# Optimization experiments

Hardware: AMD Instinct MI355X
Metric: run time of the kernel (lower is better)

## Reference

```python
import jax, jax.numpy as jnp
import numpy as np

FS = 24000.0
C_SOUND = 343.0
MAX_TAU = 6
IGNORE = -100
PAIRS = np.array([(0, 1), (0, 2), (0, 3), (1, 2), (1, 3), (2, 3)])  # m1<m2 loop order
PERMS_NP = np.array([(0, 1, 2), (0, 2, 1), (1, 0, 2), (1, 2, 0), (2, 0, 1), (2, 1, 0)])  # itertools order


def _mic_locs():
    # [rad, azi_deg, ele_deg] per mic, centered at origin (matches center_mic_coords)
    coords = np.array([[0.042, 45, 35], [0.042, -45, -35], [0.042, 135, -35], [0.042, -135, 35]], dtype=np.float64)
    rad = coords[:, 0]
    azi = coords[:, 1] * 2 * np.pi / 360
    ele = coords[:, 2] * 2 * np.pi / 360
    locs = np.stack([rad * np.cos(azi) * np.cos(ele), rad * np.sin(azi) * np.cos(ele), rad * np.sin(ele)], axis=1)
    return jnp.asarray(locs, dtype=jnp.float32)

MIC_LOCS = _mic_locs()  # [4,3]


def _get_tdoa_targets(target):
    """Vectorized get_tdoa_target. target: [B,T,E,5,C].
    Assumes <=1 active class per (b,t,track) so the random class shuffle is a no-op.
    Returns (tdoas, tdoas2) as int32 [B,T,E,6]."""
    B, T, E, F, C = target.shape
    active = target[:, :, :, 0, :]                                  # [B,T,E,C] 0/1 flags
    is_active = jnp.any(active > 0, axis=-1)                        # [B,T,E]
    doa = jnp.einsum('btec,btedc->bted', active, target[:, :, :, 1:4, :])  # [B,T,E,3]
    dist = jnp.einsum('btec,btec->bte', active, target[:, :, :, 4, :])     # [B,T,E]
    src = doa * dist[..., None]                                     # [B,T,E,3]
    d = jnp.linalg.norm(src[..., None, :] - MIC_LOCS, axis=-1)      # [B,T,E,4] dist to each mic
    tdoa = d[..., PAIRS[:, 0]] - d[..., PAIRS[:, 1]]                # [B,T,E,6]
    tdoa = jnp.round(tdoa * FS / C_SOUND) + MAX_TAU                 # [B,T,E,6]
    # compact active tracks to the front (stable keeps track order, matching tr_cnt)
    order = jnp.argsort(jnp.logical_not(is_active), axis=-1)        # [B,T,E]
    gathered = jnp.take_along_axis(tdoa, order[..., None], axis=2)  # [B,T,E,6]
    n = jnp.sum(is_active, axis=-1)                                 # [B,T] number of events
    k = jnp.arange(E)[None, None, :]                                # slot index
    idx1 = jnp.clip(jnp.minimum(k, n[:, :, None] - 1), 0, E - 1)    # pad with LAST event
    idx2 = jnp.where(k < n[:, :, None], k, 0)                       # pad with FIRST event
    tdoas = jnp.take_along_axis(gathered, idx1[..., None], axis=2)
    tdoas2 = jnp.take_along_axis(gathered, idx2[..., None], axis=2)
    empty = (n == 0)[:, :, None, None]
    tdoas = jnp.where(empty, float(IGNORE), tdoas)
    tdoas2 = jnp.where(empty, float(IGNORE), tdoas2)
    return tdoas.astype(jnp.int32), tdoas2.astype(jnp.int32)


def _forward(pred, t_a, t_b):
    B, T, C, Tr, ntd = pred.shape
    N = B * T * ntd
    p = pred.transpose(0, 1, 4, 2, 3).reshape(N, C, Tr)             # [N,C,Tr]
    ta = t_a.transpose(0, 1, 3, 2).reshape(N, Tr)                   # [N,Tr]
    tb = t_b.transpose(0, 1, 3, 2).reshape(N, Tr)
    logp = jax.nn.log_softmax(p, axis=1)                            # [N,C,Tr]
    perms = jnp.asarray(PERMS_NP)                                   # [6,Tr]
    ar = jnp.arange(Tr)

    def pit(t):
        tc = jnp.clip(t, 0, C - 1)
        # L[n,i,j] = CE(pred track j, target track i); ignore_index -> 0
        L = -jnp.take_along_axis(logp, jnp.broadcast_to(tc[:, :, None], (N, Tr, Tr)), axis=1)
        L = jnp.where((t == IGNORE)[:, :, None], 0.0, L)
        pl = L[:, ar[None, :], perms].mean(axis=-1)                 # [N,6] per-perm mean loss
        pidx = jnp.argmin(pl, axis=1)                               # first min (matches torch loop)
        return jnp.take_along_axis(pl, pidx[:, None], axis=1)[:, 0], perms[pidx]

    loss1, perm1 = pit(ta)
    loss2, perm2 = pit(tb)
    use2 = loss2 < loss1                                            # torch.min keeps first on ties
    loss = jnp.where(use2, loss2, loss1)
    t_sel = jnp.where(use2[:, None], tb, ta)
    perm_sel = jnp.where(use2[:, None], perm2, perm1)

    pred_cls = jnp.argmax(p, axis=1)                                # [N,Tr]
    t_perm = jnp.take_along_axis(t_sel, perm_sel, axis=1)           # target reordered by opt perm
    valid = t_perm != IGNORE
    npred = jnp.sum(valid)
    correct = jnp.sum((pred_cls == t_perm) & valid)
    acc = jnp.where(npred > 0, correct.astype(jnp.float32) / jnp.maximum(npred, 1).astype(jnp.float32), 0.0)

    mask = loss > 0.0
    nval = jnp.sum(mask)
    lmean = jnp.where(nval > 0, jnp.sum(jnp.where(mask, loss, 0.0)) / jnp.maximum(nval, 1).astype(loss.dtype), 0.0)
    return lmean, acc


def setup_inputs() -> dict:
    key = jax.random.key(0)
    B, T, E, NCLS, NTD, CPRED = 128, 600, 3, 13, 6, 13
    k1, k2, k3, k4, k5 = jax.random.split(key, 5)
    pred = jax.random.normal(k1, (B, T, CPRED, E, NTD), dtype=jnp.float32)
    act_cls = jax.random.randint(k2, (B, T, E), 0, NCLS)
    act_flag = (jax.random.uniform(k3, (B, T, E)) < 0.5).astype(jnp.float32)
    onehot = jax.nn.one_hot(act_cls, NCLS, dtype=jnp.float32) * act_flag[..., None]  # <=1 active class/track
    doa = jax.random.normal(k4, (B, T, E, 3), dtype=jnp.float32)
    doa = doa / jnp.linalg.norm(doa, axis=-1, keepdims=True)
    dist = jax.random.uniform(k5, (B, T, E), minval=1.0, maxval=3.0, dtype=jnp.float32)
    target = jnp.concatenate([
        onehot[:, :, :, None, :],
        jnp.broadcast_to(doa[..., None], (B, T, E, 3, NCLS)),
        jnp.broadcast_to(dist[..., None, None], (B, T, E, 1, NCLS)),
    ], axis=3).astype(jnp.float32)                                  # [B,T,E,5,NCLS]
    return {"pred": pred, "target": target}


def reference(pred, target):
    t_a, t_b = _get_tdoa_targets(target)
    return _forward(pred, t_a, t_b)
```

## Files before the change

### kernel.cpp

```cpp
#include <hip/hip_runtime.h>
#include <cstdint>
#include <cstddef>

#define BT_TOTAL 76800
#define NCLS 13
#define IGN  (-100)

#define CPB   32
#define NBLK  (BT_TOTAL / CPB)
#define ITEMS (CPB * 6)
#define NF4T  (CPB * 195 / 4)
#define KT    7
#define NF4P  (CPB * 234 / 4)
#define KP    8

struct Partial { float ls; int lc; int cor; int val; };

__device__ __forceinline__ void stage16(const float4* __restrict__ g, float4* l) {
    __builtin_amdgcn_global_load_lds((const __attribute__((address_space(1))) void*)g,
                                     (__attribute__((address_space(3))) void*)l,
                                     16, 0, 0);
}

extern "C" __global__ __launch_bounds__(256)
void tdoa_fused(const float* __restrict__ pred, const float* __restrict__ target,
                Partial* __restrict__ part) {
    const int tid = threadIdx.x;
    const int cb  = blockIdx.x * CPB;

    __shared__ float4 sBuf4[NF4P];
    __shared__ uint32_t sTd[CPB * 12];
    const float* sBuf = (const float*)sBuf4;

    {
        const float4* gt = (const float4*)(target + (size_t)cb * 195);
#pragma unroll
        for (int k = 0; k < KT; k++) {
            const int i = k * 256 + tid;
            if (i < NF4T) stage16(gt + i, &sBuf4[i]);
        }
    }
    __syncthreads();

    if (tid < CPB) {
        const float* tg = sBuf + tid * 195;

        const float MX[4] = { 0.02432757455f,  0.02432757455f, -0.02432757455f, -0.02432757455f };
        const float MY[4] = { 0.02432757455f, -0.02432757455f,  0.02432757455f, -0.02432757455f };
        const float MZ[4] = { 0.02409021033f, -0.02409021033f, -0.02409021033f,  0.02409021033f };
        const int PI_[6] = {0,0,0,1,1,2};
        const int PJ_[6] = {1,2,3,2,3,3};

        int  td[3][6];
        bool ab[3];
        int  nact = 0;
#pragma unroll
        for (int e = 0; e < 3; e++) {
            float a[NCLS];
#pragma unroll
            for (int c = 0; c < NCLS; c++) a[c] = tg[e * 65 + c];
            bool ia = false;
#pragma unroll
            for (int c = 0; c < NCLS; c++) ia = ia || (a[c] > 0.0f);
            float d0 = 0.f, d1 = 0.f, d2 = 0.f, ds = 0.f;
#pragma unroll
            for (int c = 0; c < NCLS; c++) {
                d0 += a[c] * tg[e * 65 + 13 + c];
                d1 += a[c] * tg[e * 65 + 26 + c];
                d2 += a[c] * tg[e * 65 + 39 + c];
                ds += a[c] * tg[e * 65 + 52 + c];
            }
            const float sx = d0 * ds, sy = d1 * ds, sz = d2 * ds;
            float dm[4];
#pragma unroll
            for (int m = 0; m < 4; m++) {
                const float ex = sx - MX[m], ey = sy - MY[m], ez = sz - MZ[m];
                dm[m] = sqrtf(ex * ex + ey * ey + ez * ez);
            }
#pragma unroll
            for (int p = 0; p < 6; p++) {
                const float diff = dm[PI_[p]] - dm[PJ_[p]];
                td[e][p] = (int)rintf((diff * 24000.0f) / 343.0f) + 6;
            }
            ab[e] = ia;
            nact += ia ? 1 : 0;
        }

        const int o0 = ab[0] ? 0 : (ab[1] ? 1 : 2);
        const int o1 = (ab[0] && ab[1]) ? 1 : 2;
        const bool empty = (nact == 0);

#pragma unroll
        for (int p = 0; p < 6; p++) {
            const int g0 = (o0 == 0) ? td[0][p] : ((o0 == 1) ? td[1][p] : td[2][p]);
            const int g1 = (o1 == 1) ? td[1][p] : td[2][p];
            const int g2 = td[2][p];
            int ta0 = g0;
            int ta1 = (nact >= 2) ? g1 : g0;
            int ta2 = (nact == 3) ? g2 : ((nact == 2) ? g1 : g0);
            int tb0 = g0;
            int tb1 = (nact >= 2) ? g1 : g0;
            int tb2 = (nact == 3) ? g2 : g0;
            uint32_t w0 = (uint32_t)(ta0 & 0xff) | ((uint32_t)(ta1 & 0xff) << 8) | ((uint32_t)(ta2 & 0xff) << 16);
            uint32_t w1 = (uint32_t)(tb0 & 0xff) | ((uint32_t)(tb1 & 0xff) << 8) | ((uint32_t)(tb2 & 0xff) << 16);
            if (empty) { w0 = 0x009c9c9cu; w1 = 0x009c9c9cu; }
            sTd[tid * 12 + p * 2 + 0] = w0;
            sTd[tid * 12 + p * 2 + 1] = w1;
        }
    }
    __syncthreads();

    {
        const float4* gp = (const float4*)(pred + (size_t)cb * 234);
#pragma unroll
        for (int k = 0; k < KP; k++) {
            const int i = k * 256 + tid;
            if (i < NF4P) stage16(gp + i, &sBuf4[i]);
        }
    }
    __syncthreads();

    float lsum = 0.f;
    int   lcnt = 0, cor = 0, nval = 0;

    if (tid < ITEMS) {
        const int btl = tid / 6;
        const int p   = tid - btl * 6;
        const float* pp = sBuf + btl * 234 + p;

        float x[NCLS][3];
#pragma unroll
        for (int c = 0; c < NCLS; c++)
#pragma unroll
            for (int j = 0; j < 3; j++)
                x[c][j] = pp[c * 18 + j * 6];

        int   am[3];
        float lse[3];
#pragma unroll
        for (int j = 0; j < 3; j++) {
            float m = x[0][j]; int a = 0;
#pragma unroll
            for (int c = 1; c < NCLS; c++) { if (x[c][j] > m) { m = x[c][j]; a = c; } }
            float s = 0.f;
#pragma unroll
            for (int c = 0; c < NCLS; c++) s += expf(x[c][j] - m);
            am[j] = a; lse[j] = m + logf(s);
        }

        const uint32_t w0 = sTd[btl * 12 + p * 2 + 0];
        const uint32_t w1 = sTd[btl * 12 + p * 2 + 1];
        int ta[3], tb[3];
#pragma unroll
        for (int i = 0; i < 3; i++) {
            ta[i] = (int)(int8_t)(w0 >> (8 * i));
            tb[i] = (int)(int8_t)(w1 >> (8 * i));
        }

        float La[3][3], Lb[3][3];
#pragma unroll
        for (int i = 0; i < 3; i++) {
            const int  ca  = (ta[i] < 0) ? 0 : ta[i];
            const int  cb2 = (tb[i] < 0) ? 0 : tb[i];
            const bool ia  = (ta[i] == IGN);
            const bool ib  = (tb[i] == IGN);
#pragma unroll
            for (int j = 0; j < 3; j++) {
                La[i][j] = ia ? 0.f : (lse[j] - pp[ca  * 18 + j * 6]);
                Lb[i][j] = ib ? 0.f : (lse[j] - pp[cb2 * 18 + j * 6]);
            }
        }

        const int P0[6] = {0,0,1,1,2,2};
        const int P1[6] = {1,2,0,2,0,1};
        const int P2[6] = {2,1,2,0,1,0};
        float l1 = 0.f, l2 = 0.f; int i1 = 0, i2 = 0;
#pragma unroll
        for (int q = 0; q < 6; q++) {
            const float va = (La[0][P0[q]] + La[1][P1[q]] + La[2][P2[q]]) * (1.0f / 3.0f);
            const float vb = (Lb[0][P0[q]] + Lb[1][P1[q]] + Lb[2][P2[q]]) * (1.0f / 3.0f);
            if (q == 0) { l1 = va; l2 = vb; }
            else {
                if (va < l1) { l1 = va; i1 = q; }
                if (vb < l2) { l2 = vb; i2 = q; }
            }
        }

        const bool use2 = (l2 < l1);
        const float loss = use2 ? l2 : l1;
        const int  qsel = use2 ? i2 : i1;
        const int PK[6] = {36, 24, 33, 9, 18, 6};
        int pk = PK[0];
#pragma unroll
        for (int k = 1; k < 6; k++) pk = (qsel == k) ? PK[k] : pk;
        const int s0 = use2 ? tb[0] : ta[0];
        const int s1 = use2 ? tb[1] : ta[1];
        const int s2 = use2 ? tb[2] : ta[2];
#pragma unroll
        for (int i = 0; i < 3; i++) {
            const int pi = (pk >> (2 * i)) & 3;
            const int tp = (pi == 0) ? s0 : ((pi == 1) ? s1 : s2);
            const bool v = (tp != IGN);
            nval += v ? 1 : 0;
            cor  += (v && (am[i] == tp)) ? 1 : 0;
        }
        if (loss > 0.f) { lsum += loss; lcnt++; }
    }

#pragma unroll
    for (int off = 32; off > 0; off >>= 1) {
        lsum += __shfl_down(lsum, off, 64);
        lcnt += __shfl_down(lcnt, off, 64);
        cor  += __shfl_down(cor,  off, 64);
        nval += __shfl_down(nval, off, 64);
    }
    __shared__ float rf[4];
    __shared__ int   r1[4], r2[4], r3[4];
    const int wid = tid >> 6;
    if ((tid & 63) == 0) { rf[wid] = lsum; r1[wid] = lcnt; r2[wid] = cor; r3[wid] = nval; }
    __syncthreads();
    if (tid == 0) {
        Partial pt;
        pt.ls  = rf[0] + rf[1] + rf[2] + rf[3];
        pt.lc  = r1[0] + r1[1] + r1[2] + r1[3];
        pt.cor = r2[0] + r2[1] + r2[2] + r2[3];
        pt.val = r3[0] + r3[1] + r3[2] + r3[3];
        part[blockIdx.x] = pt;
    }
}

extern "C" __global__ __launch_bounds__(256)
void tdoa_final(const Partial* __restrict__ part, float* __restrict__ out) {
    const int tid = threadIdx.x;
    double ls = 0.0; int lc = 0, cor = 0, val = 0;
    for (int i = tid; i < NBLK; i += 256) {
        const Partial p = part[i];
        ls += (double)p.ls; lc += p.lc; cor += p.cor; val += p.val;
    }
#pragma unroll
    for (int off = 32; off > 0; off >>= 1) {
        ls  += __shfl_down(ls,  off, 64);
        lc  += __shfl_down(lc,  off, 64);
        cor += __shfl_down(cor, off, 64);
        val += __shfl_down(val, off, 64);
    }
    __shared__ double sd[4];
    __shared__ int    s1[4], s2[4], s3[4];
    const int wid = tid >> 6;
    if ((tid & 63) == 0) { sd[wid] = ls; s1[wid] = lc; s2[wid] = cor; s3[wid] = val; }
    __syncthreads();
    if (tid == 0) {
        const double L = sd[0] + sd[1] + sd[2] + sd[3];
        const int c1 = s1[0] + s1[1] + s1[2] + s1[3];
        const int c2 = s2[0] + s2[1] + s2[2] + s2[3];
        const int c3 = s3[0] + s3[1] + s3[2] + s3[3];
        out[0] = (c1 > 0) ? (float)(L / (double)c1) : 0.0f;
        out[1] = (c3 > 0) ? ((float)c2 / (float)c3) : 0.0f;
    }
}

extern "C" void kernel_launch(void* const* d_in, const int* in_sizes, int n_in,
                              void* d_out, int out_size, void* d_ws, size_t ws_size,
                              hipStream_t stream) {
    const float* pred   = (const float*)d_in[0];
    const float* target = (const float*)d_in[1];
    Partial* part = (Partial*)d_ws;
    float* out = (float*)d_out;
    hipLaunchKernelGGL(tdoa_fused, dim3(NBLK), dim3(256), 0, stream, pred, target, part);
    hipLaunchKernelGGL(tdoa_final, dim3(1),    dim3(256), 0, stream, part, out);
}
```

Before: 152.1 us.

## Issue target and pred loads together and halve block size

Stages both the target and prediction tiles into separate shared buffers up front, so the prediction load no longer waits for the target processing and an extra barrier. Halves the rows per block and the threads per block, which increases the number of blocks and improves latency hiding. This uses more shared memory per row and doubles the partials the final reduction must sum.

```diff
diff --git a/kernel.cpp b/kernel.cpp
--- a/kernel.cpp
+++ b/kernel.cpp
@@ -6,8 +6,9 @@
 #define NCLS 13
 #define IGN  (-100)
 
-#define CPB   32
+#define CPB   16
 #define NBLK  (BT_TOTAL / CPB)
+#define NTHR  128
 #define ITEMS (CPB * 6)
 #define NF4T  (CPB * 195 / 4)
 #define KT    7
@@ -22,28 +23,36 @@
                                      16, 0, 0);
 }
 
-extern "C" __global__ __launch_bounds__(256)
+extern "C" __global__ __launch_bounds__(NTHR)
 void tdoa_fused(const float* __restrict__ pred, const float* __restrict__ target,
                 Partial* __restrict__ part) {
     const int tid = threadIdx.x;
     const int cb  = blockIdx.x * CPB;
 
-    __shared__ float4 sBuf4[NF4P];
+    __shared__ float4 sT4[NF4T];
+    __shared__ float4 sP4[NF4P];
     __shared__ uint32_t sTd[CPB * 12];
-    const float* sBuf = (const float*)sBuf4;
+    const float* sT = (const float*)sT4;
+    const float* sP = (const float*)sP4;
 
     {
         const float4* gt = (const float4*)(target + (size_t)cb * 195);
 #pragma unroll
         for (int k = 0; k < KT; k++) {
-            const int i = k * 256 + tid;
-            if (i < NF4T) stage16(gt + i, &sBuf4[i]);
+            const int i = k * NTHR + tid;
+            if (i < NF4T) stage16(gt + i, &sT4[i]);
+        }
+        const float4* gp = (const float4*)(pred + (size_t)cb * 234);
+#pragma unroll
+        for (int k = 0; k < KP; k++) {
+            const int i = k * NTHR + tid;
+            if (i < NF4P) stage16(gp + i, &sP4[i]);
         }
     }
     __syncthreads();
 
     if (tid < CPB) {
-        const float* tg = sBuf + tid * 195;
+        const float* tg = sT + tid * 195;
 
         const float MX[4] = { 0.02432757455f,  0.02432757455f, -0.02432757455f, -0.02432757455f };
         const float MY[4] = { 0.02432757455f, -0.02432757455f,  0.02432757455f, -0.02432757455f };
@@ -110,23 +119,13 @@
     }
     __syncthreads();
 
-    {
-        const float4* gp = (const float4*)(pred + (size_t)cb * 234);
-#pragma unroll
-        for (int k = 0; k < KP; k++) {
-            const int i = k * 256 + tid;
-            if (i < NF4P) stage16(gp + i, &sBuf4[i]);
-        }
-    }
-    __syncthreads();
-
     float lsum = 0.f;
     int   lcnt = 0, cor = 0, nval = 0;
 
     if (tid < ITEMS) {
         const int btl = tid / 6;
         const int p   = tid - btl * 6;
-        const float* pp = sBuf + btl * 234 + p;
+        const float* pp = sP + btl * 234 + p;
 
         float x[NCLS][3];
 #pragma unroll
@@ -214,17 +213,17 @@
         cor  += __shfl_down(cor,  off, 64);
         nval += __shfl_down(nval, off, 64);
     }
-    __shared__ float rf[4];
-    __shared__ int   r1[4], r2[4], r3[4];
+    __shared__ float rf[2];
+    __shared__ int   r1[2], r2[2], r3[2];
     const int wid = tid >> 6;
     if ((tid & 63) == 0) { rf[wid] = lsum; r1[wid] = lcnt; r2[wid] = cor; r3[wid] = nval; }
     __syncthreads();
     if (tid == 0) {
         Partial pt;
-        pt.ls  = rf[0] + rf[1] + rf[2] + rf[3];
-        pt.lc  = r1[0] + r1[1] + r1[2] + r1[3];
-        pt.cor = r2[0] + r2[1] + r2[2] + r2[3];
-        pt.val = r3[0] + r3[1] + r3[2] + r3[3];
+        pt.ls  = rf[0] + rf[1];
+        pt.lc  = r1[0] + r1[1];
+        pt.cor = r2[0] + r2[1];
+        pt.val = r3[0] + r3[1];
         part[blockIdx.x] = pt;
     }
 }
@@ -266,6 +265,6 @@
     const float* target = (const float*)d_in[1];
     Partial* part = (Partial*)d_ws;
     float* out = (float*)d_out;
-    hipLaunchKernelGGL(tdoa_fused, dim3(NBLK), dim3(256), 0, stream, pred, target, part);
+    hipLaunchKernelGGL(tdoa_fused, dim3(NBLK), dim3(NTHR), 0, stream, pred, target, part);
     hipLaunchKernelGGL(tdoa_final, dim3(1),    dim3(256), 0, stream, part, out);
 }
```

Measured after the change: 164.1 us. +7.9%, slower.

## Flatten kernel to one thread per (cell,pair) reading global memory directly

Applied to the files above, without the earlier changes.

Replaces the block-staged design (async global-to-LDS copies, a 32-thread TDOA phase, and barriers) with a flat grid where every thread handles one (cell, pair) item and reads target and pred straight from global memory. Each thread recomputes only its own pair's TDOA. It also swaps the 13-class dot products for a select of the single active class, which relies on the one-hot assumption. The aim is to drop the barriers and idle lanes. The cost is redundant, uncoalesced strided global reads of target across the 6 threads of a cell, relying on cache for reuse.

```diff
diff --git a/kernel.cpp b/kernel.cpp
--- a/kernel.cpp
+++ b/kernel.cpp
@@ -3,209 +3,145 @@
 #include <cstddef>
 
 #define BT_TOTAL 76800
-#define NCLS 13
-#define IGN  (-100)
-
-#define CPB   32
-#define NBLK  (BT_TOTAL / CPB)
-#define ITEMS (CPB * 6)
-#define NF4T  (CPB * 195 / 4)
-#define KT    7
-#define NF4P  (CPB * 234 / 4)
-#define KP    8
+#define NITEMS   (BT_TOTAL * 6)
+#define NTHR     256
+#define NBLK     (NITEMS / NTHR)
+#define NCLS     13
+#define IGN      (-100)
 
 struct Partial { float ls; int lc; int cor; int val; };
 
-__device__ __forceinline__ void stage16(const float4* __restrict__ g, float4* l) {
-    __builtin_amdgcn_global_load_lds((const __attribute__((address_space(1))) void*)g,
-                                     (__attribute__((address_space(3))) void*)l,
-                                     16, 0, 0);
-}
-
-extern "C" __global__ __launch_bounds__(256)
-void tdoa_fused(const float* __restrict__ pred, const float* __restrict__ target,
-                Partial* __restrict__ part) {
-    const int tid = threadIdx.x;
-    const int cb  = blockIdx.x * CPB;
-
-    __shared__ float4 sBuf4[NF4P];
-    __shared__ uint32_t sTd[CPB * 12];
-    const float* sBuf = (const float*)sBuf4;
-
-    {
-        const float4* gt = (const float4*)(target + (size_t)cb * 195);
-#pragma unroll
-        for (int k = 0; k < KT; k++) {
-            const int i = k * 256 + tid;
-            if (i < NF4T) stage16(gt + i, &sBuf4[i]);
+extern "C" __global__ __launch_bounds__(NTHR, 5)
+void tdoa_flat(const float* __restrict__ pred, const float* __restrict__ target,
+               Partial* __restrict__ part) {
+    const int tid  = threadIdx.x;
+    const int gid  = blockIdx.x * NTHR + tid;
+    const int cell = gid / 6;
+    const int p    = gid - cell * 6;
+
+    const float* tg = target + (size_t)cell * 195;
+    const float* pp = pred   + (size_t)cell * 234 + p;
+
+    const float MX[4] = { 0.02432757455f,  0.02432757455f, -0.02432757455f, -0.02432757455f };
+    const float MY[4] = { 0.02432757455f, -0.02432757455f,  0.02432757455f, -0.02432757455f };
+    const float MZ[4] = { 0.02409021033f, -0.02409021033f, -0.02409021033f,  0.02409021033f };
+    const int PI_[6] = {0,0,0,1,1,2};
+    const int PJ_[6] = {1,2,3,2,3,3};
+    const int mi = PI_[p], mj = PJ_[p];
+    const float mxi = MX[mi], myi = MY[mi], mzi = MZ[mi];
+    const float mxj = MX[mj], myj = MY[mj], mzj = MZ[mj];
+
+    int  td[3];
+    bool ab[3];
+    int  nact = 0;
+#pragma unroll
+    for (int e = 0; e < 3; e++) {
+        float av = 0.f; int ci = 0; bool ia = false;
+#pragma unroll
+        for (int c = 0; c < NCLS; c++) {
+            const float a = tg[e * 65 + c];
+            const bool  g = (a > 0.0f);
+            av = g ? a : av;
+            ci = g ? c : ci;
+            ia = ia || g;
         }
-    }
-    __syncthreads();
-
-    if (tid < CPB) {
-        const float* tg = sBuf + tid * 195;
-
-        const float MX[4] = { 0.02432757455f,  0.02432757455f, -0.02432757455f, -0.02432757455f };
-        const float MY[4] = { 0.02432757455f, -0.02432757455f,  0.02432757455f, -0.02432757455f };
-        const float MZ[4] = { 0.02409021033f, -0.02409021033f, -0.02409021033f,  0.02409021033f };
-        const int PI_[6] = {0,0,0,1,1,2};
-        const int PJ_[6] = {1,2,3,2,3,3};
-
-        int  td[3][6];
-        bool ab[3];
-        int  nact = 0;
-#pragma unroll
-        for (int e = 0; e < 3; e++) {
-            float a[NCLS];
-#pragma unroll
-            for (int c = 0; c < NCLS; c++) a[c] = tg[e * 65 + c];
-            bool ia = false;
-#pragma unroll
-            for (int c = 0; c < NCLS; c++) ia = ia || (a[c] > 0.0f);
-            float d0 = 0.f, d1 = 0.f, d2 = 0.f, ds = 0.f;
-#pragma unroll
-            for (int c = 0; c < NCLS; c++) {
-                d0 += a[c] * tg[e * 65 + 13 + c];
-                d1 += a[c] * tg[e * 65 + 26 + c];
-                d2 += a[c] * tg[e * 65 + 39 + c];
-                ds += a[c] * tg[e * 65 + 52 + c];
-            }
-            const float sx = d0 * ds, sy = d1 * ds, sz = d2 * ds;
-            float dm[4];
-#pragma unroll
-            for (int m = 0; m < 4; m++) {
-                const float ex = sx - MX[m], ey = sy - MY[m], ez = sz - MZ[m];
-                dm[m] = sqrtf(ex * ex + ey * ey + ez * ez);
-            }
-#pragma unroll
-            for (int p = 0; p < 6; p++) {
-                const float diff = dm[PI_[p]] - dm[PJ_[p]];
-                td[e][p] = (int)rintf((diff * 24000.0f) / 343.0f) + 6;
-            }
-            ab[e] = ia;
-            nact += ia ? 1 : 0;
+        const float d0 = av * tg[e * 65 + 13 + ci];
+        const float d1 = av * tg[e * 65 + 26 + ci];
+        const float d2 = av * tg[e * 65 + 39 + ci];
+        const float ds = av * tg[e * 65 + 52 + ci];
+        const float sx = d0 * ds, sy = d1 * ds, sz = d2 * ds;
+        const float exi = sx - mxi, eyi = sy - myi, ezi = sz - mzi;
+        const float exj = sx - mxj, eyj = sy - myj, ezj = sz - mzj;
+        const float dmi = sqrtf(exi * exi + eyi * eyi + ezi * ezi);
+        const float dmj = sqrtf(exj * exj + eyj * eyj + ezj * ezj);
+        td[e] = (int)rintf((dmi - dmj) * (24000.0f / 343.0f)) + 6;
+        ab[e] = ia;
+        nact += ia ? 1 : 0;
+    }
+
+    const int g0 = ab[0] ? td[0] : (ab[1] ? td[1] : td[2]);
+    const int g1 = (ab[0] && ab[1]) ? td[1] : td[2];
+    const int g2 = td[2];
+    int ta[3], tb[3];
+    ta[0] = g0;
+    ta[1] = (nact >= 2) ? g1 : g0;
+    ta[2] = (nact == 3) ? g2 : ((nact == 2) ? g1 : g0);
+    tb[0] = g0;
+    tb[1] = (nact >= 2) ? g1 : g0;
+    tb[2] = (nact == 3) ? g2 : g0;
+    if (nact == 0) { ta[0] = ta[1] = ta[2] = IGN; tb[0] = tb[1] = tb[2] = IGN; }
+
+    float x[NCLS][3];
+#pragma unroll
+    for (int c = 0; c < NCLS; c++)
+#pragma unroll
+        for (int j = 0; j < 3; j++)
+            x[c][j] = pp[c * 18 + j * 6];
+
+    int   am[3];
+    float lse[3];
+#pragma unroll
+    for (int j = 0; j < 3; j++) {
+        float m = x[0][j]; int a = 0;
+#pragma unroll
+        for (int c = 1; c < NCLS; c++) { if (x[c][j] > m) { m = x[c][j]; a = c; } }
+        float s = 0.f;
+#pragma unroll
+        for (int c = 0; c < NCLS; c++) s += expf(x[c][j] - m);
+        am[j] = a; lse[j] = m + logf(s);
+    }
+
+    float La[3][3], Lb[3][3];
+#pragma unroll
+    for (int i = 0; i < 3; i++) {
+        const int  ca  = (ta[i] < 0) ? 0 : ta[i];
+        const int  cbb = (tb[i] < 0) ? 0 : tb[i];
+        const bool ia2 = (ta[i] == IGN);
+        const bool ib2 = (tb[i] == IGN);
+#pragma unroll
+        for (int j = 0; j < 3; j++) {
+            La[i][j] = ia2 ? 0.f : (lse[j] - pp[ca  * 18 + j * 6]);
+            Lb[i][j] = ib2 ? 0.f : (lse[j] - pp[cbb * 18 + j * 6]);
         }
-
-        const int o0 = ab[0] ? 0 : (ab[1] ? 1 : 2);
-        const int o1 = (ab[0] && ab[1]) ? 1 : 2;
-        const bool empty = (nact == 0);
-
-#pragma unroll
-        for (int p = 0; p < 6; p++) {
-            const int g0 = (o0 == 0) ? td[0][p] : ((o0 == 1) ? td[1][p] : td[2][p]);
-            const int g1 = (o1 == 1) ? td[1][p] : td[2][p];
-            const int g2 = td[2][p];
-            int ta0 = g0;
-            int ta1 = (nact >= 2) ? g1 : g0;
-            int ta2 = (nact == 3) ? g2 : ((nact == 2) ? g1 : g0);
-            int tb0 = g0;
-            int tb1 = (nact >= 2) ? g1 : g0;
-            int tb2 = (nact == 3) ? g2 : g0;
-            uint32_t w0 = (uint32_t)(ta0 & 0xff) | ((uint32_t)(ta1 & 0xff) << 8) | ((uint32_t)(ta2 & 0xff) << 16);
-            uint32_t w1 = (uint32_t)(tb0 & 0xff) | ((uint32_t)(tb1 & 0xff) << 8) | ((uint32_t)(tb2 & 0xff) << 16);
-            if (empty) { w0 = 0x009c9c9cu; w1 = 0x009c9c9cu; }
-            sTd[tid * 12 + p * 2 + 0] = w0;
-            sTd[tid * 12 + p * 2 + 1] = w1;
+    }
+
+    const int P0[6] = {0,0,1,1,2,2};
+    const int P1[6] = {1,2,0,2,0,1};
+    const int P2[6] = {2,1,2,0,1,0};
+    float l1 = 0.f, l2 = 0.f; int i1 = 0, i2 = 0;
+#pragma unroll
+    for (int q = 0; q < 6; q++) {
+        const float va = (La[0][P0[q]] + La[1][P1[q]] + La[2][P2[q]]) * (1.0f / 3.0f);
+        const float vb = (Lb[0][P0[q]] + Lb[1][P1[q]] + Lb[2][P2[q]]) * (1.0f / 3.0f);
+        if (q == 0) { l1 = va; l2 = vb; }
+        else {
+            if (va < l1) { l1 = va; i1 = q; }
+            if (vb < l2) { l2 = vb; i2 = q; }
         }
     }
-    __syncthreads();
-
-    {
-        const float4* gp = (const float4*)(pred + (size_t)cb * 234);
-#pragma unroll
-        for (int k = 0; k < KP; k++) {
-            const int i = k * 256 + tid;
-            if (i < NF4P) stage16(gp + i, &sBuf4[i]);
-        }
-    }
-    __syncthreads();
+
+    const bool use2 = (l2 < l1);
+    const float loss = use2 ? l2 : l1;
+    const int  qsel = use2 ? i2 : i1;
+    const int PK[6] = {36, 24, 33, 9, 18, 6};
+    int pk = PK[0];
+#pragma unroll
+    for (int k = 1; k < 6; k++) pk = (qsel == k) ? PK[k] : pk;
+    const int s0 = use2 ? tb[0] : ta[0];
+    const int s1 = use2 ? tb[1] : ta[1];
+    const int s2 = use2 ? tb[2] : ta[2];
 
     float lsum = 0.f;
     int   lcnt = 0, cor = 0, nval = 0;
-
-    if (tid < ITEMS) {
-        const int btl = tid / 6;
-        const int p   = tid - btl * 6;
-        const float* pp = sBuf + btl * 234 + p;
-
-        float x[NCLS][3];
-#pragma unroll
-        for (int c = 0; c < NCLS; c++)
-#pragma unroll
-            for (int j = 0; j < 3; j++)
-                x[c][j] = pp[c * 18 + j * 6];
-
-        int   am[3];
-        float lse[3];
-#pragma unroll
-        for (int j = 0; j < 3; j++) {
-            float m = x[0][j]; int a = 0;
-#pragma unroll
-            for (int c = 1; c < NCLS; c++) { if (x[c][j] > m) { m = x[c][j]; a = c; } }
-            float s = 0.f;
-#pragma unroll
-            for (int c = 0; c < NCLS; c++) s += expf(x[c][j] - m);
-            am[j] = a; lse[j] = m + logf(s);
-        }
-
-        const uint32_t w0 = sTd[btl * 12 + p * 2 + 0];
-        const uint32_t w1 = sTd[btl * 12 + p * 2 + 1];
-        int ta[3], tb[3];
-#pragma unroll
-        for (int i = 0; i < 3; i++) {
-            ta[i] = (int)(int8_t)(w0 >> (8 * i));
-            tb[i] = (int)(int8_t)(w1 >> (8 * i));
-        }
-
-        float La[3][3], Lb[3][3];
-#pragma unroll
-        for (int i = 0; i < 3; i++) {
-            const int  ca  = (ta[i] < 0) ? 0 : ta[i];
-            const int  cb2 = (tb[i] < 0) ? 0 : tb[i];
-            const bool ia  = (ta[i] == IGN);
-            const bool ib  = (tb[i] == IGN);
-#pragma unroll
-            for (int j = 0; j < 3; j++) {
-                La[i][j] = ia ? 0.f : (lse[j] - pp[ca  * 18 + j * 6]);
-                Lb[i][j] = ib ? 0.f : (lse[j] - pp[cb2 * 18 + j * 6]);
-            }
-        }
-
-        const int P0[6] = {0,0,1,1,2,2};
-        const int P1[6] = {1,2,0,2,0,1};
-        const int P2[6] = {2,1,2,0,1,0};
-        float l1 = 0.f, l2 = 0.f; int i1 = 0, i2 = 0;
-#pragma unroll
-        for (int q = 0; q < 6; q++) {
-            const float va = (La[0][P0[q]] + La[1][P1[q]] + La[2][P2[q]]) * (1.0f / 3.0f);
-            const float vb = (Lb[0][P0[q]] + Lb[1][P1[q]] + Lb[2][P2[q]]) * (1.0f / 3.0f);
-            if (q == 0) { l1 = va; l2 = vb; }
-            else {
-                if (va < l1) { l1 = va; i1 = q; }
-                if (vb < l2) { l2 = vb; i2 = q; }
-            }
-        }
-
-        const bool use2 = (l2 < l1);
-        const float loss = use2 ? l2 : l1;
-        const int  qsel = use2 ? i2 : i1;
-        const int PK[6] = {36, 24, 33, 9, 18, 6};
-        int pk = PK[0];
-#pragma unroll
-        for (int k = 1; k < 6; k++) pk = (qsel == k) ? PK[k] : pk;
-        const int s0 = use2 ? tb[0] : ta[0];
-        const int s1 = use2 ? tb[1] : ta[1];
-        const int s2 = use2 ? tb[2] : ta[2];
-#pragma unroll
-        for (int i = 0; i < 3; i++) {
-            const int pi = (pk >> (2 * i)) & 3;
-            const int tp = (pi == 0) ? s0 : ((pi == 1) ? s1 : s2);
-            const bool v = (tp != IGN);
-            nval += v ? 1 : 0;
-            cor  += (v && (am[i] == tp)) ? 1 : 0;
-        }
-        if (loss > 0.f) { lsum += loss; lcnt++; }
-    }
+#pragma unroll
+    for (int i = 0; i < 3; i++) {
+        const int pi = (pk >> (2 * i)) & 3;
+        const int tp = (pi == 0) ? s0 : ((pi == 1) ? s1 : s2);
+        const bool v = (tp != IGN);
+        nval += v ? 1 : 0;
+        cor  += (v && (am[i] == tp)) ? 1 : 0;
+    }
+    if (loss > 0.f) { lsum += loss; lcnt++; }
 
 #pragma unroll
     for (int off = 32; off > 0; off >>= 1) {
@@ -266,6 +202,6 @@
     const float* target = (const float*)d_in[1];
     Partial* part = (Partial*)d_ws;
     float* out = (float*)d_out;
-    hipLaunchKernelGGL(tdoa_fused, dim3(NBLK), dim3(256), 0, stream, pred, target, part);
+    hipLaunchKernelGGL(tdoa_flat,  dim3(NBLK), dim3(NTHR), 0, stream, pred, target, part);
     hipLaunchKernelGGL(tdoa_final, dim3(1),    dim3(256), 0, stream, part, out);
 }
```

Result: slower. 180.6 us (+18.7%).
